# Performance work log

Hardware: AMD Instinct MI355X
Metric: run time of the kernel (lower is better)

The kernel has to match this reference:

```python
import jax, jax.numpy as jnp
import numpy as np

B, T, D = 32, 512, 512


def setup_inputs() -> dict:
    key = jax.random.key(0)
    kx, kd = jax.random.split(key)
    x = jax.random.normal(kx, (B, T, D), dtype=jnp.float32)
    dur = jax.random.randint(kd, (B, T), 0, 8, dtype=jnp.int64)
    return {"x": x, "dur": dur}


def reference(x, dur):
    # x: [B, T, D] encoder features; dur: [B, T] integer durations (frames per token)
    dur = jnp.maximum(dur, 0)                      # duration[duration < 0] = 0
    tot = jnp.cumsum(dur, axis=1)                  # [B, T] cumulative end positions
    max_duration = int(jnp.max(tot[:, -1]))        # padded expanded length (eager concretization)
    frames = jnp.arange(max_duration)              # [M]
    # frame t maps to first token j with cumsum > t (zero-duration tokens are skipped);
    # frames past a row's total map past T and are clipped to the last token (matches
    # the original's trailing fill with j = T-1).
    idx = jax.vmap(lambda row: jnp.searchsorted(row, frames, side='right'))(tot)  # [B, M]
    idx = jnp.clip(idx, 0, x.shape[1] - 1)
    return jnp.take_along_axis(x, idx[:, :, None], axis=1)  # [B, M, D]
```

## Files before the change

### kernel.cpp

```cpp
#include <hip/hip_runtime.h>


#define B_BATCH 32
#define T_TOK   512
#define D_DIM   512
#define DQ      (D_DIM / 4)

__global__ void lr_scan_scatter(const int* __restrict__ dur,
                                int* __restrict__ idx, int M) {
    __shared__ int s[T_TOK];
    const int b = blockIdx.x;
    const int t = threadIdx.x;

    int d = dur[b * T_TOK + t];
    if (d < 0) d = 0;

    for (int m = t; m < M; m += T_TOK) idx[b * M + m] = T_TOK - 1;

    s[t] = d;
    __syncthreads();
    #pragma unroll
    for (int off = 1; off < T_TOK; off <<= 1) {
        int v = (t >= off) ? s[t - off] : 0;
        __syncthreads();
        s[t] += v;
        __syncthreads();
    }
    const int tot = s[t];
    for (int p = tot - d; p < tot; ++p) idx[b * M + p] = t;
}

__global__ void lr_gather(const float4* __restrict__ x,
                          const int* __restrict__ idx,
                          float4* __restrict__ out, int M) {
    const int b = blockIdx.y;
    const int e = blockIdx.x * blockDim.x + threadIdx.x;
    const int QM = M * DQ;
    if (e >= QM) return;
    const int m   = e >> 7;
    const int q   = e & (DQ - 1);
    const int row = idx[b * M + m];
    out[(size_t)b * QM + e] = x[((size_t)b * T_TOK + row) * DQ + q];
}

extern "C" void kernel_launch(void* const* d_in, const int* in_sizes, int n_in,
                              void* d_out, int out_size, void* d_ws, size_t ws_size,
                              hipStream_t stream) {
    const float* x  = (const float*)d_in[0];
    const int* dur  = (const int*)d_in[1];
    float* out      = (float*)d_out;

    const int M = out_size / (B_BATCH * D_DIM);
    int* idx = (int*)d_ws;

    lr_scan_scatter<<<B_BATCH, T_TOK, 0, stream>>>(dur, idx, M);

    const int QM = M * DQ;
    dim3 grid((QM + 255) / 256, B_BATCH);
    lr_gather<<<grid, 256, 0, stream>>>((const float4*)x, idx, (float4*)out, M);
}
```

Measured before the change: 158.6 us.

## Replace per-frame index gather with per-token replicate-write expansion

The scan kernel now writes only per-token start offsets and per-row totals instead of scattering a full frame-to-token index array. The expand kernel assigns one 128-thread group per token: it reads the token's row of x once and writes it d times to consecutive output frames. A separate set of blocks fills the tail past each row's total with the last token. This removes the index array writes and reads and the repeated reads of x, at the cost of uneven per-thread work because durations vary.

After: 153.7 us. 1.03x faster.

```diff
diff --git a/kernel.cpp b/kernel.cpp
--- a/kernel.cpp
+++ b/kernel.cpp
@@ -5,17 +5,18 @@
 #define T_TOK   512
 #define D_DIM   512
 #define DQ      (D_DIM / 4)
+#define TPB     4
+#define TAILB   32
 
-__global__ void lr_scan_scatter(const int* __restrict__ dur,
-                                int* __restrict__ idx, int M) {
+__global__ __launch_bounds__(T_TOK)
+void lr_scan(const int* __restrict__ dur,
+             int* __restrict__ start, int* __restrict__ total) {
     __shared__ int s[T_TOK];
     const int b = blockIdx.x;
     const int t = threadIdx.x;
 
     int d = dur[b * T_TOK + t];
     if (d < 0) d = 0;
-
-    for (int m = t; m < M; m += T_TOK) idx[b * M + m] = T_TOK - 1;
 
     s[t] = d;
     __syncthreads();
@@ -27,35 +28,53 @@
         __syncthreads();
     }
     const int tot = s[t];
-    for (int p = tot - d; p < tot; ++p) idx[b * M + p] = t;
+    start[b * T_TOK + t] = tot - d;
+    if (t == T_TOK - 1) total[b] = tot;
 }
 
-__global__ void lr_gather(const float4* __restrict__ x,
-                          const int* __restrict__ idx,
-                          float4* __restrict__ out, int M) {
-    const int b = blockIdx.y;
-    const int e = blockIdx.x * blockDim.x + threadIdx.x;
-    const int QM = M * DQ;
-    if (e >= QM) return;
-    const int m   = e >> 7;
-    const int q   = e & (DQ - 1);
-    const int row = idx[b * M + m];
-    out[(size_t)b * QM + e] = x[((size_t)b * T_TOK + row) * DQ + q];
+__global__ __launch_bounds__(2 * T_TOK > 512 ? 512 : 512)
+void lr_expand(const float4* __restrict__ x,
+               const int* __restrict__ dur,
+               const int* __restrict__ start,
+               const int* __restrict__ total,
+               float4* __restrict__ out, int M) {
+    const int b   = blockIdx.y;
+    const int q   = threadIdx.x & (DQ - 1);
+    const int sub = threadIdx.x >> 7;
+
+    if (blockIdx.x < T_TOK / TPB) {
+        const int t = blockIdx.x * TPB + sub;
+        int d = dur[b * T_TOK + t];
+        if (d <= 0) return;
+        const float4 v = x[((size_t)b * T_TOK + t) * DQ + q];
+        const int st = start[b * T_TOK + t];
+        float4* o = out + ((size_t)b * M + st) * DQ + q;
+        for (int k = 0; k < d; ++k) o[k * DQ] = v;
+    } else {
+        const int tot = total[b];
+        if (tot >= M) return;
+        const float4 v = x[((size_t)b * T_TOK + (T_TOK - 1)) * DQ + q];
+        const int j = blockIdx.x - T_TOK / TPB;
+        for (int r = tot + j * TPB + sub; r < M; r += TAILB * TPB)
+            out[((size_t)b * M + r) * DQ + q] = v;
+    }
 }
 
 extern "C" void kernel_launch(void* const* d_in, const int* in_sizes, int n_in,
                               void* d_out, int out_size, void* d_ws, size_t ws_size,
                               hipStream_t stream) {
-    const float* x  = (const float*)d_in[0];
-    const int* dur  = (const int*)d_in[1];
-    float* out      = (float*)d_out;
+    const float* x = (const float*)d_in[0];
+    const int* dur = (const int*)d_in[1];
+    float* out     = (float*)d_out;
 
     const int M = out_size / (B_BATCH * D_DIM);
-    int* idx = (int*)d_ws;
 
-    lr_scan_scatter<<<B_BATCH, T_TOK, 0, stream>>>(dur, idx, M);
+    int* start = (int*)d_ws;
+    int* total = start + B_BATCH * T_TOK;
 
-    const int QM = M * DQ;
-    dim3 grid((QM + 255) / 256, B_BATCH);
-    lr_gather<<<grid, 256, 0, stream>>>((const float4*)x, idx, (float4*)out, M);
+    lr_scan<<<B_BATCH, T_TOK, 0, stream>>>(dur, start, total);
+
+    dim3 grid(T_TOK / TPB + TAILB, B_BATCH);
+    lr_expand<<<grid, TPB * DQ, 0, stream>>>((const float4*)x, dur, start, total,
+                                             (float4*)out, M);
 }
```
